# Kernel tuning notes

Measured on AMD Instinct MI355X. Metric: run time of the kernel, lower is better.

## Reference

```python
import jax, jax.numpy as jnp
import numpy as np

B, C, H, W = 8, 32, 256, 448


def setup_inputs() -> dict:
    key = jax.random.key(0)
    k1, k2 = jax.random.split(key)
    input1 = jax.random.normal(k1, (B, C, H, W), dtype=jnp.float32)
    input2 = jax.random.normal(k2, (B, 2, H, W), dtype=jnp.float32)  # flow (u, v)
    return {"input1": input1, "input2": input2, "kernel_size": 1}


def _forward_splat(input1, input2):
    """Forward warp: splat each source pixel to (x+u, y+v) with bilinear weights,
    accumulating via scatter-add (kernel_size=1 -> 2x2 bilinear footprint)."""
    b, c, h, w = input1.shape
    u = input2[:, 0]  # [B,H,W] horizontal flow
    v = input2[:, 1]  # [B,H,W] vertical flow
    xs = jnp.arange(w, dtype=input2.dtype)
    ys = jnp.arange(h, dtype=input2.dtype)
    tx = xs[None, None, :] + u  # target x, [B,H,W]
    ty = ys[None, :, None] + v  # target y, [B,H,W]
    x0 = jnp.floor(tx).astype(jnp.int32)
    y0 = jnp.floor(ty).astype(jnp.int32)
    fx = tx - x0.astype(tx.dtype)
    fy = ty - y0.astype(ty.dtype)

    vals = input1.transpose(0, 2, 3, 1).reshape(b * h * w, c)  # [BHW, C]
    out = jnp.zeros((b * h * w, c), dtype=input1.dtype)
    batch_off = (jnp.arange(b, dtype=jnp.int32) * (h * w))[:, None, None]

    for dx, dy in ((0, 0), (1, 0), (0, 1), (1, 1)):
        xx = x0 + dx
        yy = y0 + dy
        wx = fx if dx == 1 else (1.0 - fx)
        wy = fy if dy == 1 else (1.0 - fy)
        wgt = wx * wy  # [B,H,W]
        valid = (xx >= 0) & (xx < w) & (yy >= 0) & (yy < h)
        wgt = jnp.where(valid, wgt, 0.0)
        idx = batch_off + jnp.clip(yy, 0, h - 1) * w + jnp.clip(xx, 0, w - 1)
        out = out.at[idx.reshape(-1)].add(wgt.reshape(-1, 1) * vals)

    return out.reshape(b, h, w, c).transpose(0, 3, 1, 2)


def reference(input1, input2, kernel_size):
    # kernel_size=1 corresponds to the standard bilinear (2x2) splat footprint.
    return _forward_splat(input1, input2)
```

## Files before the change

### kernel.cpp

```cpp
#include <hip/hip_runtime.h>
#include <hip/hip_fp16.h>

constexpr int B = 8;
constexpr int C = 32;
constexpr int H = 256;
constexpr int W = 448;
constexpr int HW = H * W;

constexpr int TW  = 64;
constexpr int TH  = 8;
constexpr int RAD = 3;
constexpr int WXV = 72;
constexpr int WY  = TH + 2 * RAD;
constexpr int NV  = WXV * WY;
constexpr int NT  = 512;
constexpr int GITER = (NV + NT - 1) / NT;
constexpr int NG4 = (WXV / 4) * WY;
constexpr int NITEM = NG4 * 8;
constexpr int KITER = (NITEM + NT - 1) / NT;

static __device__ __forceinline__ unsigned pkrtz(float a, float b) {
    return __builtin_bit_cast(unsigned, __builtin_amdgcn_cvt_pkrtz(a, b));
}

static __device__ __forceinline__ __half2 h2(unsigned u) {
    union { unsigned u; __half2 h; } x;
    x.u = u;
    return x.h;
}

__global__ __launch_bounds__(NT)
void splat_out(const float* __restrict__ in1,
               const float* __restrict__ flow,
               float* __restrict__ out,
               unsigned* __restrict__ wcnt,
               unsigned* __restrict__ wlist,
               unsigned cap) {
    __shared__ unsigned long long mAllS[NT];
    __shared__ unsigned char     geomR8[NV];
    __shared__ uint2             geomW[NV];
    __shared__ __align__(16) uint2 valV2[8 * NV];

    int bid = blockIdx.x;
    int b = bid & 7;
    int t = bid >> 3;
    int ty = t / 7;
    int tx = t - ty * 7;
    int ox = tx * TW, oy = ty * TH;
    int tid = threadIdx.x;
    int qlx = tid & 63, qly = tid >> 6;
    int qx = ox + qlx, qy = oy + qly;

    mAllS[tid] = 0ull;
    __syncthreads();

    const int fbase = b * 2 * HW;
#pragma unroll
    for (int k = 0; k < GITER; ++k) {
        int i = tid + k * NT;
        if (i < NV) {
            int wy = i / WXV, wv = i - wy * WXV;
            int gx = ox + wv - 4;
            int sy = oy + wy - RAD;
            uint2 wd = make_uint2(0u, 0u);
            unsigned gr = 0xFFu;
            if ((unsigned)gx < (unsigned)W && (unsigned)sy < (unsigned)H) {
                int g = sy * W + gx;
                float u = flow[fbase + g];
                float v = flow[fbase + g + HW];
                float txf = (float)gx + u;
                float tyf = (float)sy + v;
                float x0f = floorf(txf), y0f = floorf(tyf);
                int rx = (int)x0f - gx, ry = (int)y0f - sy;
                if (rx >= -RAD && rx <= RAD - 1 && ry >= -RAD && ry <= RAD - 1) {
                    float fx = txf - x0f, fy = tyf - y0f;
                    wd.x = pkrtz((1.f - fx) * (1.f - fy), fx * (1.f - fy));
                    wd.y = pkrtz((1.f - fx) * fy,         fx * fy);
                    gr = (unsigned)(rx + RAD) | ((unsigned)(ry + RAD) << 3);
#pragma unroll
                    for (int corner = 0; corner < 4; ++corner) {
                        int dxx = corner & 1, dyy = corner >> 1;
                        int ccx = gx + rx + dxx - ox;
                        int ccy = sy + ry + dyy - oy;
                        if ((unsigned)ccx < (unsigned)TW &&
                            (unsigned)ccy < (unsigned)TH) {
                            int cell = ccy * TW + ccx;
                            unsigned long long bit =
                                1ull << ((3 - (ry + dyy)) * 8 + (3 - (rx + dxx)));
                            atomicOr(&mAllS[cell], bit);
                        }
                    }
                } else if (wv >= 4 && wv < 4 + TW &&
                           wy >= RAD && wy < RAD + TH) {
                    unsigned slot = atomicAdd(wcnt, 1u);
                    if (slot < cap) wlist[slot] = ((unsigned)b << 17) | (unsigned)g;
                }
            }
            geomR8[i] = (unsigned char)gr;
            geomW[i]  = wd;
        }
    }

    const float* inb = in1 + (size_t)b * C * HW;
#pragma unroll
    for (int k = 0; k < KITER; ++k) {
        int id = tid + k * NT;
        if (id < NITEM) {
            int g4 = id % NG4;
            int pp = id / NG4;
            int wy = g4 / (WXV / 4);
            int wv4 = (g4 - wy * (WXV / 4)) * 4;
            int row = min(max(oy + wy - RAD, 0), H - 1);
            int gxb = min(max(ox + wv4 - 4, 0), W - 4);
            const float* base = inb + (size_t)(4 * pp) * HW
                                    + (size_t)row * W + gxb;
            float4 c0 = *reinterpret_cast<const float4*>(base);
            float4 c1 = *reinterpret_cast<const float4*>(base + (size_t)HW);
            float4 c2 = *reinterpret_cast<const float4*>(base + (size_t)2 * HW);
            float4 c3 = *reinterpret_cast<const float4*>(base + (size_t)3 * HW);
            int vbase = pp * NV + wy * WXV + wv4;
            uint4* dst = reinterpret_cast<uint4*>(&valV2[vbase]);
            uint4 w0, w1;
            w0.x = pkrtz(c0.x, c1.x); w0.y = pkrtz(c2.x, c3.x);
            w0.z = pkrtz(c0.y, c1.y); w0.w = pkrtz(c2.y, c3.y);
            w1.x = pkrtz(c0.z, c1.z); w1.y = pkrtz(c2.z, c3.z);
            w1.z = pkrtz(c0.w, c1.w); w1.w = pkrtz(c2.w, c3.w);
            dst[0] = w0;
            dst[1] = w1;
        }
    }
    __syncthreads();

    const unsigned long long m0 = mAllS[tid];
    const int qbase = (qly + RAD) * WXV + (qlx + 4);
    float* outp = out + (size_t)b * C * HW + qy * W + qx;

    __half2 acc2[16];
#pragma unroll
    for (int k = 0; k < 16; ++k) acc2[k] = h2(0u);

    unsigned long long m = m0;
    while (m) {
        int j = (int)__builtin_ctzll(m);
        m &= m - 1;
        int wi = qbase + ((j >> 3) - 3) * WXV + ((j & 7) - 3);
        unsigned g8 = geomR8[wi];
        unsigned dxx = 6u - (unsigned)(j & 7) - (g8 & 7u);
        unsigned dyy = 6u - (unsigned)(j >> 3) - (g8 >> 3);
        uint2 wd2 = geomW[wi];
        unsigned wd = dyy ? wd2.y : wd2.x;
        unsigned hq = (wd >> (16u * dxx)) & 0xFFFFu;
        __half2 w2 = h2(hq | (hq << 16));
#pragma unroll
        for (int pp = 0; pp < 8; ++pp) {
            uint2 vv = valV2[pp * NV + wi];
            acc2[2 * pp + 0] = __hfma2(h2(vv.x), w2, acc2[2 * pp + 0]);
            acc2[2 * pp + 1] = __hfma2(h2(vv.y), w2, acc2[2 * pp + 1]);
        }
    }

#pragma unroll
    for (int pp = 0; pp < 8; ++pp) {
        float2 f01 = __half22float2(acc2[2 * pp + 0]);
        float2 f23 = __half22float2(acc2[2 * pp + 1]);
        outp[(size_t)(4 * pp + 0) * HW] = f01.x;
        outp[(size_t)(4 * pp + 1) * HW] = f01.y;
        outp[(size_t)(4 * pp + 2) * HW] = f23.x;
        outp[(size_t)(4 * pp + 3) * HW] = f23.y;
    }
}

__global__ void outlier_combined(const float* __restrict__ in1,
                                 const float* __restrict__ flow,
                                 float* __restrict__ out,
                                 const unsigned* __restrict__ wcnt,
                                 const unsigned* __restrict__ wlist,
                                 unsigned cap) {
    unsigned n = *wcnt;
    if (n <= cap) {
        unsigned total = n * 8u;
        for (unsigned idx = blockIdx.x * blockDim.x + threadIdx.x;
             idx < total; idx += gridDim.x * blockDim.x) {
            unsigned e = wlist[idx >> 3];
            int c0 = (int)(idx & 7u) * 4;
            int bb = (int)(e >> 17);
            int p  = (int)(e & 0x1FFFFu);
            int y = p / W, x = p - y * W;

            float u = flow[(bb * 2 + 0) * HW + p];
            float v = flow[(bb * 2 + 1) * HW + p];
            float txf = (float)x + u;
            float tyf = (float)y + v;
            float fx0 = floorf(txf), fy0 = floorf(tyf);
            int x0 = (int)fx0, y0 = (int)fy0;
            float fx = txf - fx0, fy = tyf - fy0;
            float w00 = (1.0f - fx) * (1.0f - fy);
            float w10 = fx * (1.0f - fy);
            float w01 = (1.0f - fx) * fy;
            float w11 = fx * fy;
            bool vx0 = (x0 >= 0) && (x0 < W);
            bool vx1 = (x0 + 1 >= 0) && (x0 + 1 < W);
            bool vy0 = (y0 >= 0) && (y0 < H);
            bool vy1 = (y0 + 1 >= 0) && (y0 + 1 < H);
            long o00 = (long)y0 * W + x0;

            const float* src  = in1 + (size_t)bb * C * HW + (size_t)c0 * HW + p;
            float*       dstb = out + (size_t)bb * C * HW + (size_t)c0 * HW;
            for (int c = 0; c < 4; ++c) {
                float val = src[(size_t)c * HW];
                float* ob = dstb + (size_t)c * HW;
                if (vx0 && vy0) atomicAdd(ob + o00,         w00 * val);
                if (vx1 && vy0) atomicAdd(ob + o00 + 1,     w10 * val);
                if (vx0 && vy1) atomicAdd(ob + o00 + W,     w01 * val);
                if (vx1 && vy1) atomicAdd(ob + o00 + W + 1, w11 * val);
            }
        }
    } else {
        int npix = B * HW;
        for (int idx = blockIdx.x * blockDim.x + threadIdx.x;
             idx < npix; idx += gridDim.x * blockDim.x) {
            int b = idx / HW;
            int p = idx - b * HW;
            int y = p / W, x = p - y * W;
            float u = flow[(b * 2 + 0) * HW + p];
            float v = flow[(b * 2 + 1) * HW + p];
            float txf = (float)x + u;
            float tyf = (float)y + v;
            float fx0 = floorf(txf), fy0 = floorf(tyf);
            int x0 = (int)fx0, y0 = (int)fy0;
            int rx = x0 - x, ry = y0 - y;
            bool handled = (rx >= -RAD) && (rx <= RAD - 1) &&
                           (ry >= -RAD) && (ry <= RAD - 1);
            if (handled) continue;
            float fx = txf - fx0, fy = tyf - fy0;
            float w00 = (1.0f - fx) * (1.0f - fy);
            float w10 = fx * (1.0f - fy);
            float w01 = (1.0f - fx) * fy;
            float w11 = fx * fy;
            bool vx0 = (x0 >= 0) && (x0 < W);
            bool vx1 = (x0 + 1 >= 0) && (x0 + 1 < W);
            bool vy0 = (y0 >= 0) && (y0 < H);
            bool vy1 = (y0 + 1 >= 0) && (y0 + 1 < H);
            long o00 = (long)y0 * W + x0;
            const float* src = in1 + (size_t)b * C * HW + p;
            float* dstb = out + (size_t)b * C * HW;
            for (int c = 0; c < C; ++c) {
                float val = src[(size_t)c * HW];
                float* ob = dstb + (size_t)c * HW;
                if (vx0 && vy0) atomicAdd(ob + o00,         w00 * val);
                if (vx1 && vy0) atomicAdd(ob + o00 + 1,     w10 * val);
                if (vx0 && vy1) atomicAdd(ob + o00 + W,     w01 * val);
                if (vx1 && vy1) atomicAdd(ob + o00 + W + 1, w11 * val);
            }
        }
    }
}

extern "C" void kernel_launch(void* const* d_in, const int* in_sizes, int n_in,
                              void* d_out, int out_size, void* d_ws, size_t ws_size,
                              hipStream_t stream) {
    const float* in1  = (const float*)d_in[0];
    const float* flow = (const float*)d_in[1];
    float* out = (float*)d_out;

    unsigned* wcnt  = (unsigned*)d_ws;
    unsigned* wlist = wcnt + 4;
    unsigned cap = 0;
    if (ws_size >= 64) {
        size_t c = ws_size / sizeof(unsigned) - 4;
        cap = (c > 0x7FFFFFFFull) ? 0x7FFFFFFFu : (unsigned)c;
    }

    hipMemsetAsync(wcnt, 0, sizeof(unsigned), stream);

    int nblocks = B * (H / TH) * (W / TW);
    splat_out<<<nblocks, NT, 0, stream>>>(in1, flow, out, wcnt, wlist, cap);

    outlier_combined<<<256, 256, 0, stream>>>(in1, flow, out, wcnt, wlist, cap);
}
```

Before: 108.4 us.

## Split channel staging into two halves with register prefetch overlapping compute

Channel values are now staged through shared memory in two 16-channel halves instead of all 32 at once, which halves the LDS footprint for values. The first half's global loads are issued into registers before the flow/geometry pass so they overlap it. The second half's loads are issued before the first gather so they overlap it. The cost is extra register pressure (two sets of float4 prefetch buffers), two extra barriers, and running the mask loop and weight decode twice.

```diff
diff --git a/kernel.cpp b/kernel.cpp
--- a/kernel.cpp
+++ b/kernel.cpp
@@ -16,8 +16,8 @@
 constexpr int NT  = 512;
 constexpr int GITER = (NV + NT - 1) / NT;
 constexpr int NG4 = (WXV / 4) * WY;
-constexpr int NITEM = NG4 * 8;
-constexpr int KITER = (NITEM + NT - 1) / NT;
+constexpr int NITEM16 = NG4 * 4;
+constexpr int KIT16 = (NITEM16 + NT - 1) / NT;
 
 static __device__ __forceinline__ unsigned pkrtz(float a, float b) {
     return __builtin_bit_cast(unsigned, __builtin_amdgcn_cvt_pkrtz(a, b));
@@ -39,7 +39,7 @@
     __shared__ unsigned long long mAllS[NT];
     __shared__ unsigned char     geomR8[NV];
     __shared__ uint2             geomW[NV];
-    __shared__ __align__(16) uint2 valV2[8 * NV];
+    __shared__ __align__(16) uint2 valV2[4 * NV];
 
     int bid = blockIdx.x;
     int b = bid & 7;
@@ -50,6 +50,40 @@
     int tid = threadIdx.x;
     int qlx = tid & 63, qly = tid >> 6;
     int qx = ox + qlx, qy = oy + qly;
+
+    const float* inb = in1 + (size_t)b * C * HW;
+
+    int sOff[KIT16];
+    int sVb[KIT16];
+    int sPp[KIT16];
+#pragma unroll
+    for (int k = 0; k < KIT16; ++k) {
+        int id = tid + k * NT;
+        if (id < NITEM16) {
+            int g4 = id % NG4;
+            int pp = id / NG4;
+            int wy = g4 / (WXV / 4);
+            int wv4 = (g4 - wy * (WXV / 4)) * 4;
+            int row = min(max(oy + wy - RAD, 0), H - 1);
+            int gxb = min(max(ox + wv4 - 4, 0), W - 4);
+            sOff[k] = row * W + gxb;
+            sVb[k]  = pp * NV + wy * WXV + wv4;
+            sPp[k]  = pp;
+        } else {
+            sOff[k] = -1; sVb[k] = 0; sPp[k] = 0;
+        }
+    }
+
+    float4 r0[KIT16][4];
+#pragma unroll
+    for (int k = 0; k < KIT16; ++k) {
+        if (sOff[k] >= 0) {
+            const float* base = inb + (size_t)(4 * sPp[k]) * HW + sOff[k];
+#pragma unroll
+            for (int c = 0; c < 4; ++c)
+                r0[k][c] = *reinterpret_cast<const float4*>(base + (size_t)c * HW);
+        }
+    }
 
     mAllS[tid] = 0ull;
     __syncthreads();
@@ -101,30 +135,15 @@
         }
     }
 
-    const float* inb = in1 + (size_t)b * C * HW;
-#pragma unroll
-    for (int k = 0; k < KITER; ++k) {
-        int id = tid + k * NT;
-        if (id < NITEM) {
-            int g4 = id % NG4;
-            int pp = id / NG4;
-            int wy = g4 / (WXV / 4);
-            int wv4 = (g4 - wy * (WXV / 4)) * 4;
-            int row = min(max(oy + wy - RAD, 0), H - 1);
-            int gxb = min(max(ox + wv4 - 4, 0), W - 4);
-            const float* base = inb + (size_t)(4 * pp) * HW
-                                    + (size_t)row * W + gxb;
-            float4 c0 = *reinterpret_cast<const float4*>(base);
-            float4 c1 = *reinterpret_cast<const float4*>(base + (size_t)HW);
-            float4 c2 = *reinterpret_cast<const float4*>(base + (size_t)2 * HW);
-            float4 c3 = *reinterpret_cast<const float4*>(base + (size_t)3 * HW);
-            int vbase = pp * NV + wy * WXV + wv4;
-            uint4* dst = reinterpret_cast<uint4*>(&valV2[vbase]);
+#pragma unroll
+    for (int k = 0; k < KIT16; ++k) {
+        if (sOff[k] >= 0) {
+            uint4* dst = reinterpret_cast<uint4*>(&valV2[sVb[k]]);
             uint4 w0, w1;
-            w0.x = pkrtz(c0.x, c1.x); w0.y = pkrtz(c2.x, c3.x);
-            w0.z = pkrtz(c0.y, c1.y); w0.w = pkrtz(c2.y, c3.y);
-            w1.x = pkrtz(c0.z, c1.z); w1.y = pkrtz(c2.z, c3.z);
-            w1.z = pkrtz(c0.w, c1.w); w1.w = pkrtz(c2.w, c3.w);
+            w0.x = pkrtz(r0[k][0].x, r0[k][1].x); w0.y = pkrtz(r0[k][2].x, r0[k][3].x);
+            w0.z = pkrtz(r0[k][0].y, r0[k][1].y); w0.w = pkrtz(r0[k][2].y, r0[k][3].y);
+            w1.x = pkrtz(r0[k][0].z, r0[k][1].z); w1.y = pkrtz(r0[k][2].z, r0[k][3].z);
+            w1.z = pkrtz(r0[k][0].w, r0[k][1].w); w1.w = pkrtz(r0[k][2].w, r0[k][3].w);
             dst[0] = w0;
             dst[1] = w1;
         }
@@ -135,39 +154,70 @@
     const int qbase = (qly + RAD) * WXV + (qlx + 4);
     float* outp = out + (size_t)b * C * HW + qy * W + qx;
 
-    __half2 acc2[16];
-#pragma unroll
-    for (int k = 0; k < 16; ++k) acc2[k] = h2(0u);
-
-    unsigned long long m = m0;
-    while (m) {
-        int j = (int)__builtin_ctzll(m);
-        m &= m - 1;
-        int wi = qbase + ((j >> 3) - 3) * WXV + ((j & 7) - 3);
-        unsigned g8 = geomR8[wi];
-        unsigned dxx = 6u - (unsigned)(j & 7) - (g8 & 7u);
-        unsigned dyy = 6u - (unsigned)(j >> 3) - (g8 >> 3);
-        uint2 wd2 = geomW[wi];
-        unsigned wd = dyy ? wd2.y : wd2.x;
-        unsigned hq = (wd >> (16u * dxx)) & 0xFFFFu;
-        __half2 w2 = h2(hq | (hq << 16));
-#pragma unroll
-        for (int pp = 0; pp < 8; ++pp) {
-            uint2 vv = valV2[pp * NV + wi];
-            acc2[2 * pp + 0] = __hfma2(h2(vv.x), w2, acc2[2 * pp + 0]);
-            acc2[2 * pp + 1] = __hfma2(h2(vv.y), w2, acc2[2 * pp + 1]);
-        }
-    }
-
-#pragma unroll
-    for (int pp = 0; pp < 8; ++pp) {
-        float2 f01 = __half22float2(acc2[2 * pp + 0]);
-        float2 f23 = __half22float2(acc2[2 * pp + 1]);
-        outp[(size_t)(4 * pp + 0) * HW] = f01.x;
-        outp[(size_t)(4 * pp + 1) * HW] = f01.y;
-        outp[(size_t)(4 * pp + 2) * HW] = f23.x;
-        outp[(size_t)(4 * pp + 3) * HW] = f23.y;
-    }
+    float4 r1[KIT16][4];
+#pragma unroll
+    for (int k = 0; k < KIT16; ++k) {
+        if (sOff[k] >= 0) {
+            const float* base = inb + (size_t)(16 + 4 * sPp[k]) * HW + sOff[k];
+#pragma unroll
+            for (int c = 0; c < 4; ++c)
+                r1[k][c] = *reinterpret_cast<const float4*>(base + (size_t)c * HW);
+        }
+    }
+
+    auto gather16 = [&](float* o) {
+        __half2 acc2[8];
+#pragma unroll
+        for (int k = 0; k < 8; ++k) acc2[k] = h2(0u);
+        unsigned long long m = m0;
+        while (m) {
+            int j = (int)__builtin_ctzll(m);
+            m &= m - 1;
+            int wi = qbase + ((j >> 3) - 3) * WXV + ((j & 7) - 3);
+            unsigned g8 = geomR8[wi];
+            unsigned dxx = 6u - (unsigned)(j & 7) - (g8 & 7u);
+            unsigned dyy = 6u - (unsigned)(j >> 3) - (g8 >> 3);
+            uint2 wd2 = geomW[wi];
+            unsigned wd = dyy ? wd2.y : wd2.x;
+            unsigned hq = (wd >> (16u * dxx)) & 0xFFFFu;
+            __half2 w2 = h2(hq | (hq << 16));
+#pragma unroll
+            for (int pp = 0; pp < 4; ++pp) {
+                uint2 vv = valV2[pp * NV + wi];
+                acc2[2 * pp + 0] = __hfma2(h2(vv.x), w2, acc2[2 * pp + 0]);
+                acc2[2 * pp + 1] = __hfma2(h2(vv.y), w2, acc2[2 * pp + 1]);
+            }
+        }
+#pragma unroll
+        for (int pp = 0; pp < 4; ++pp) {
+            float2 f01 = __half22float2(acc2[2 * pp + 0]);
+            float2 f23 = __half22float2(acc2[2 * pp + 1]);
+            o[(size_t)(4 * pp + 0) * HW] = f01.x;
+            o[(size_t)(4 * pp + 1) * HW] = f01.y;
+            o[(size_t)(4 * pp + 2) * HW] = f23.x;
+            o[(size_t)(4 * pp + 3) * HW] = f23.y;
+        }
+    };
+
+    gather16(outp);
+    __syncthreads();
+
+#pragma unroll
+    for (int k = 0; k < KIT16; ++k) {
+        if (sOff[k] >= 0) {
+            uint4* dst = reinterpret_cast<uint4*>(&valV2[sVb[k]]);
+            uint4 w0, w1;
+            w0.x = pkrtz(r1[k][0].x, r1[k][1].x); w0.y = pkrtz(r1[k][2].x, r1[k][3].x);
+            w0.z = pkrtz(r1[k][0].y, r1[k][1].y); w0.w = pkrtz(r1[k][2].y, r1[k][3].y);
+            w1.x = pkrtz(r1[k][0].z, r1[k][1].z); w1.y = pkrtz(r1[k][2].z, r1[k][3].z);
+            w1.z = pkrtz(r1[k][0].w, r1[k][1].w); w1.w = pkrtz(r1[k][2].w, r1[k][3].w);
+            dst[0] = w0;
+            dst[1] = w1;
+        }
+    }
+    __syncthreads();
+
+    gather16(outp + (size_t)16 * HW);
 }
 
 __global__ void outlier_combined(const float* __restrict__ in1,
```

Measured after the change: 107.9 us (median of 2 runs). Within noise of the previous version (-0.4%).

## Double tile height and stage channels in two 16-channel passes

Applied to the files above, without the earlier changes.

Raises the tile from 64x8 to 64x16 output pixels per block, with each thread handling two rows. Input values are staged into shared memory in two passes of 16 channels instead of one pass of all 32. The goal is to cut the halo overhead per output pixel (rows 8+6 become 16+6) and keep shared memory bounded. The costs are an extra pair of barriers, a second gather loop, divergence from interleaving two bitmasks per thread, and half as many blocks in the grid. The grid launch and the other kernels are not shown, so the diff may be incomplete if they are not updated to match.

```diff
diff --git a/kernel.cpp b/kernel.cpp
--- a/kernel.cpp
+++ b/kernel.cpp
@@ -8,16 +8,17 @@
 constexpr int HW = H * W;
 
 constexpr int TW  = 64;
-constexpr int TH  = 8;
+constexpr int TH  = 16;
 constexpr int RAD = 3;
 constexpr int WXV = 72;
 constexpr int WY  = TH + 2 * RAD;
 constexpr int NV  = WXV * WY;
 constexpr int NT  = 512;
+constexpr int CELLS = TW * TH;
 constexpr int GITER = (NV + NT - 1) / NT;
 constexpr int NG4 = (WXV / 4) * WY;
-constexpr int NITEM = NG4 * 8;
-constexpr int KITER = (NITEM + NT - 1) / NT;
+constexpr int NITEM16 = NG4 * 4;
+constexpr int KIT16 = (NITEM16 + NT - 1) / NT;
 
 static __device__ __forceinline__ unsigned pkrtz(float a, float b) {
     return __builtin_bit_cast(unsigned, __builtin_amdgcn_cvt_pkrtz(a, b));
@@ -36,10 +37,10 @@
                unsigned* __restrict__ wcnt,
                unsigned* __restrict__ wlist,
                unsigned cap) {
-    __shared__ unsigned long long mAllS[NT];
+    __shared__ unsigned long long mAllS[CELLS];
     __shared__ unsigned char     geomR8[NV];
     __shared__ uint2             geomW[NV];
-    __shared__ __align__(16) uint2 valV2[8 * NV];
+    __shared__ __align__(16) uint2 valV2[4 * NV];
 
     int bid = blockIdx.x;
     int b = bid & 7;
@@ -51,7 +52,8 @@
     int qlx = tid & 63, qly = tid >> 6;
     int qx = ox + qlx, qy = oy + qly;
 
-    mAllS[tid] = 0ull;
+    mAllS[tid]       = 0ull;
+    mAllS[tid + NT]  = 0ull;
     __syncthreads();
 
     const int fbase = b * 2 * HW;
@@ -102,72 +104,104 @@
     }
 
     const float* inb = in1 + (size_t)b * C * HW;
-#pragma unroll
-    for (int k = 0; k < KITER; ++k) {
-        int id = tid + k * NT;
-        if (id < NITEM) {
-            int g4 = id % NG4;
-            int pp = id / NG4;
-            int wy = g4 / (WXV / 4);
-            int wv4 = (g4 - wy * (WXV / 4)) * 4;
-            int row = min(max(oy + wy - RAD, 0), H - 1);
-            int gxb = min(max(ox + wv4 - 4, 0), W - 4);
-            const float* base = inb + (size_t)(4 * pp) * HW
-                                    + (size_t)row * W + gxb;
-            float4 c0 = *reinterpret_cast<const float4*>(base);
-            float4 c1 = *reinterpret_cast<const float4*>(base + (size_t)HW);
-            float4 c2 = *reinterpret_cast<const float4*>(base + (size_t)2 * HW);
-            float4 c3 = *reinterpret_cast<const float4*>(base + (size_t)3 * HW);
-            int vbase = pp * NV + wy * WXV + wv4;
-            uint4* dst = reinterpret_cast<uint4*>(&valV2[vbase]);
-            uint4 w0, w1;
-            w0.x = pkrtz(c0.x, c1.x); w0.y = pkrtz(c2.x, c3.x);
-            w0.z = pkrtz(c0.y, c1.y); w0.w = pkrtz(c2.y, c3.y);
-            w1.x = pkrtz(c0.z, c1.z); w1.y = pkrtz(c2.z, c3.z);
-            w1.z = pkrtz(c0.w, c1.w); w1.w = pkrtz(c2.w, c3.w);
-            dst[0] = w0;
-            dst[1] = w1;
-        }
-    }
+
+    auto stage16 = [&](int pass) {
+#pragma unroll
+        for (int k = 0; k < KIT16; ++k) {
+            int id = tid + k * NT;
+            if (id < NITEM16) {
+                int g4 = id % NG4;
+                int pp = id / NG4;
+                int wy = g4 / (WXV / 4);
+                int wv4 = (g4 - wy * (WXV / 4)) * 4;
+                int row = min(max(oy + wy - RAD, 0), H - 1);
+                int gxb = min(max(ox + wv4 - 4, 0), W - 4);
+                const float* base = inb + (size_t)(16 * pass + 4 * pp) * HW
+                                        + (size_t)row * W + gxb;
+                float4 c0 = *reinterpret_cast<const float4*>(base);
+                float4 c1 = *reinterpret_cast<const float4*>(base + (size_t)HW);
+                float4 c2 = *reinterpret_cast<const float4*>(base + (size_t)2 * HW);
+                float4 c3 = *reinterpret_cast<const float4*>(base + (size_t)3 * HW);
+                int vbase = pp * NV + wy * WXV + wv4;
+                uint4* dst = reinterpret_cast<uint4*>(&valV2[vbase]);
+                uint4 w0, w1;
+                w0.x = pkrtz(c0.x, c1.x); w0.y = pkrtz(c2.x, c3.x);
+                w0.z = pkrtz(c0.y, c1.y); w0.w = pkrtz(c2.y, c3.y);
+                w1.x = pkrtz(c0.z, c1.z); w1.y = pkrtz(c2.z, c3.z);
+                w1.z = pkrtz(c0.w, c1.w); w1.w = pkrtz(c2.w, c3.w);
+                dst[0] = w0;
+                dst[1] = w1;
+            }
+        }
+    };
+
+    stage16(0);
     __syncthreads();
 
-    const unsigned long long m0 = mAllS[tid];
-    const int qbase = (qly + RAD) * WXV + (qlx + 4);
+    const int qbA = (qly + RAD) * WXV + (qlx + 4);
+    const int qbB = (qly + 8 + RAD) * WXV + (qlx + 4);
     float* outp = out + (size_t)b * C * HW + qy * W + qx;
 
-    __half2 acc2[16];
-#pragma unroll
-    for (int k = 0; k < 16; ++k) acc2[k] = h2(0u);
-
-    unsigned long long m = m0;
-    while (m) {
-        int j = (int)__builtin_ctzll(m);
-        m &= m - 1;
-        int wi = qbase + ((j >> 3) - 3) * WXV + ((j & 7) - 3);
-        unsigned g8 = geomR8[wi];
-        unsigned dxx = 6u - (unsigned)(j & 7) - (g8 & 7u);
-        unsigned dyy = 6u - (unsigned)(j >> 3) - (g8 >> 3);
-        uint2 wd2 = geomW[wi];
-        unsigned wd = dyy ? wd2.y : wd2.x;
-        unsigned hq = (wd >> (16u * dxx)) & 0xFFFFu;
-        __half2 w2 = h2(hq | (hq << 16));
-#pragma unroll
-        for (int pp = 0; pp < 8; ++pp) {
-            uint2 vv = valV2[pp * NV + wi];
-            acc2[2 * pp + 0] = __hfma2(h2(vv.x), w2, acc2[2 * pp + 0]);
-            acc2[2 * pp + 1] = __hfma2(h2(vv.y), w2, acc2[2 * pp + 1]);
-        }
-    }
-
-#pragma unroll
-    for (int pp = 0; pp < 8; ++pp) {
-        float2 f01 = __half22float2(acc2[2 * pp + 0]);
-        float2 f23 = __half22float2(acc2[2 * pp + 1]);
-        outp[(size_t)(4 * pp + 0) * HW] = f01.x;
-        outp[(size_t)(4 * pp + 1) * HW] = f01.y;
-        outp[(size_t)(4 * pp + 2) * HW] = f23.x;
-        outp[(size_t)(4 * pp + 3) * HW] = f23.y;
-    }
+    auto gather16 = [&](float* oA) {
+        __half2 aA[8], aB[8];
+#pragma unroll
+        for (int k = 0; k < 8; ++k) { aA[k] = h2(0u); aB[k] = h2(0u); }
+        unsigned long long mA = mAllS[tid];
+        unsigned long long mB = mAllS[tid + NT];
+        while (mA | mB) {
+            bool useB = (mA == 0ull);
+            unsigned long long mm = useB ? mB : mA;
+            int j = (int)__builtin_ctzll(mm);
+            mm &= mm - 1;
+            if (useB) mB = mm; else mA = mm;
+            int qb = useB ? qbB : qbA;
+            int wi = qb + ((j >> 3) - 3) * WXV + ((j & 7) - 3);
+            unsigned g8 = geomR8[wi];
+            unsigned dxx = 6u - (unsigned)(j & 7) - (g8 & 7u);
+            unsigned dyy = 6u - (unsigned)(j >> 3) - (g8 >> 3);
+            uint2 wd2 = geomW[wi];
+            unsigned wd = dyy ? wd2.y : wd2.x;
+            unsigned hq = (wd >> (16u * dxx)) & 0xFFFFu;
+            __half2 w2 = h2(hq | (hq << 16));
+            if (useB) {
+#pragma unroll
+                for (int pp = 0; pp < 4; ++pp) {
+                    uint2 vv = valV2[pp * NV + wi];
+                    aB[2 * pp + 0] = __hfma2(h2(vv.x), w2, aB[2 * pp + 0]);
+                    aB[2 * pp + 1] = __hfma2(h2(vv.y), w2, aB[2 * pp + 1]);
+                }
+            } else {
+#pragma unroll
+                for (int pp = 0; pp < 4; ++pp) {
+                    uint2 vv = valV2[pp * NV + wi];
+                    aA[2 * pp + 0] = __hfma2(h2(vv.x), w2, aA[2 * pp + 0]);
+                    aA[2 * pp + 1] = __hfma2(h2(vv.y), w2, aA[2 * pp + 1]);
+                }
+            }
+        }
+        float* oB = oA + (size_t)8 * W;
+#pragma unroll
+        for (int pp = 0; pp < 4; ++pp) {
+            float2 a01 = __half22float2(aA[2 * pp + 0]);
+            float2 a23 = __half22float2(aA[2 * pp + 1]);
+            float2 b01 = __half22float2(aB[2 * pp + 0]);
+            float2 b23 = __half22float2(aB[2 * pp + 1]);
+            oA[(size_t)(4 * pp + 0) * HW] = a01.x;
+            oA[(size_t)(4 * pp + 1) * HW] = a01.y;
+            oA[(size_t)(4 * pp + 2) * HW] = a23.x;
+            oA[(size_t)(4 * pp + 3) * HW] = a23.y;
+            oB[(size_t)(4 * pp + 0) * HW] = b01.x;
+            oB[(size_t)(4 * pp + 1) * HW] = b01.y;
+            oB[(size_t)(4 * pp + 2) * HW] = b23.x;
+            oB[(size_t)(4 * pp + 3) * HW] = b23.y;
+        }
+    };
+
+    gather16(outp);
+    __syncthreads();
+    stage16(1);
+    __syncthreads();
+    gather16(outp + (size_t)16 * HW);
 }
 
 __global__ void outlier_combined(const float* __restrict__ in1,
```

Result: slower. 121.8 us (+12.4%).
